# Kernel tuning notes

Hardware: AMD Instinct MI355X
Metric: run time of the kernel (lower is better)

Reference implementation:

```python
import jax, jax.numpy as jnp
import numpy as np
import math

B, N, DEG, C, F0, NCLS = 128, 512, 8, 128, 128, 10
E = B * N * DEG
RATIO = 0.8
K1 = math.ceil(RATIO * N)    # 410
K2 = math.ceil(RATIO * K1)   # 328
K3 = math.ceil(RATIO * K2)   # 263


def setup_inputs() -> dict:
    key = jax.random.key(0)
    ks = jax.random.split(key, 32)
    x = jax.random.normal(ks[0], (B * N, F0), jnp.float32)
    epg = N * DEG
    src_l = jax.random.randint(ks[1], (B, epg), 0, N)
    dst_l = jax.random.randint(ks[2], (B, epg), 0, N)
    off = (jnp.arange(B, dtype=jnp.int32) * N)[:, None]
    edge_src = (src_l + off).reshape(-1).astype(jnp.int32)
    edge_dst = (dst_l + off).reshape(-1).astype(jnp.int32)

    def lin(k, fi, fo):
        return jax.random.normal(k, (fi, fo), jnp.float32) / np.float32(np.sqrt(fi))

    inp = {"x": x, "edge_src": edge_src, "edge_dst": edge_dst}
    i = 3
    for s, fi in (("1", F0), ("2", C), ("3", C)):
        inp["Wroot" + s] = lin(ks[i], fi, C); i += 1
        inp["Wrel" + s] = lin(ks[i], fi, C); i += 1
        inp["brel" + s] = jnp.zeros((C,), jnp.float32)
        inp["p" + s] = jax.random.normal(ks[i], (C,), jnp.float32); i += 1
    inp["W1"] = lin(ks[i], 2 * C, 128); i += 1
    inp["b1"] = jnp.zeros((128,), jnp.float32)
    inp["W2"] = lin(ks[i], 128, 64); i += 1
    inp["b2"] = jnp.zeros((64,), jnp.float32)
    inp["W3"] = lin(ks[i], 64, NCLS); i += 1
    inp["b3"] = jnp.zeros((NCLS,), jnp.float32)
    return inp


def graph_conv(x, src, dst, emask, Wroot, Wrel, brel, num_nodes):
    # PyG GraphConv (aggr='add'): lin_rel(sum_j x_j) + lin_root(x_i)
    msg = x[src] * emask[:, None]                      # masked gather  [E, C]
    agg = jax.ops.segment_sum(msg, dst, num_segments=num_nodes)
    return agg @ Wrel + brel + x @ Wroot


def topk_pool(x, p, src, dst, emask, b, n, k):
    # score = tanh(x . p / ||p||), keep top-k nodes per graph, scale kept x by score
    score = jnp.tanh((x @ p) / jnp.linalg.norm(p))     # [b*n]
    vals, idx = jax.lax.top_k(score.reshape(b, n), k)  # [b, k]
    perm = (idx + (jnp.arange(b, dtype=idx.dtype) * n)[:, None]).reshape(-1)
    x_new = x[perm] * vals.reshape(-1, 1)
    inv = jnp.full((b * n,), -1, jnp.int32).at[perm].set(
        jnp.arange(b * k, dtype=jnp.int32))
    ns, nd = inv[src], inv[dst]
    nmask = emask * (ns >= 0) * (nd >= 0)
    return x_new, jnp.maximum(ns, 0), jnp.maximum(nd, 0), nmask


def readout(h, b, k):
    hb = h.reshape(b, k, -1)
    return jnp.concatenate([hb.max(axis=1), hb.mean(axis=1)], axis=-1)  # gmp||gap


def reference(x, edge_src, edge_dst,
              Wroot1, Wrel1, brel1, p1,
              Wroot2, Wrel2, brel2, p2,
              Wroot3, Wrel3, brel3, p3,
              W1, b1, W2, b2, W3, b3):
    emask = jnp.ones((E,), x.dtype)
    s, d = edge_src, edge_dst

    h = jax.nn.relu(graph_conv(x, s, d, emask, Wroot1, Wrel1, brel1, B * N))
    h, s, d, emask = topk_pool(h, p1, s, d, emask, B, N, K1)
    x1 = readout(h, B, K1)

    h = jax.nn.relu(graph_conv(h, s, d, emask, Wroot2, Wrel2, brel2, B * K1))
    h, s, d, emask = topk_pool(h, p2, s, d, emask, B, K1, K2)
    x2 = readout(h, B, K2)

    h = jax.nn.relu(graph_conv(h, s, d, emask, Wroot3, Wrel3, brel3, B * K2))
    h, s, d, emask = topk_pool(h, p3, s, d, emask, B, K2, K3)
    x3 = readout(h, B, K3)

    g = x1 + x2 + x3                                   # [B, 256]
    g = jax.nn.relu(g @ W1 + b1)                       # dropout is identity in eval
    g = jax.nn.relu(g @ W2 + b2)
    return jax.nn.log_softmax(g @ W3 + b3, axis=-1)    # [B, NCLS]
```

## Files before the change

kernel.cpp:

```cpp
#include <hip/hip_runtime.h>
#include <hip/hip_bf16.h>
#include <math.h>

#define B_G   128
#define N0    512
#define DEG   8
#define CCH   128
#define EPG   (N0*DEG)
#define E_TOTAL (B_G*EPG)
#define K1    410
#define K2    328
#define K3    263
#define NCLS  10

using bf16x8 = __attribute__((ext_vector_type(8))) __bf16;
using f32x4  = __attribute__((ext_vector_type(4))) float;
typedef unsigned short ushort;
typedef unsigned int uint;

__device__ __forceinline__ ushort f2b(float f) {
    uint u = __float_as_uint(f);
    u += 0x7fffu + ((u >> 16) & 1u);
    return (ushort)(u >> 16);
}
__device__ __forceinline__ float b2f(ushort h) {
    return __uint_as_float(((uint)h) << 16);
}
__device__ __forceinline__ void split2(float v, ushort& hi, ushort& lo) {
    hi = f2b(v);
    lo = f2b(v - b2f(hi));
}
__device__ __forceinline__ uint pksplit(float v) {
    ushort h, l; split2(v, h, l);
    return (uint)h | ((uint)l << 16);
}
__device__ __forceinline__ float unpk(uint u) {
    return __uint_as_float(u << 16) + __uint_as_float(u & 0xffff0000u);
}
__device__ __forceinline__ float keyval(unsigned long long key) {
    uint tu = (uint)(key >> 32);
    uint su = (tu & 0x80000000u) ? (tu & 0x7fffffffu) : ~tu;
    return __uint_as_float(su);
}

__global__ __launch_bounds__(512) void setup_kernel(
        const float* __restrict__ Wrel0, const float* __restrict__ Wroot0,
        const float* __restrict__ Wrel1, const float* __restrict__ Wroot1,
        const float* __restrict__ Wrel2, const float* __restrict__ Wroot2,
        ushort* __restrict__ Bph, ushort* __restrict__ Bpl,
        const int* __restrict__ es, const int* __restrict__ ed,
        int* __restrict__ indptr0, int* __restrict__ counts0, ushort* __restrict__ srclist0) {
    __shared__ uint epk[EPG];
    __shared__ int cnt[512], pref[512], curs[512];
    if (blockIdx.x < B_G) {
        int b = blockIdx.x, tid = threadIdx.x;
        cnt[tid] = 0;
        __syncthreads();
        int base = b * EPG;
        for (int i = tid; i < EPG; i += 512) {
            int s = es[base + i] & (N0 - 1);
            int d = ed[base + i] & (N0 - 1);
            epk[i] = (uint)s | ((uint)d << 16);
            atomicAdd(&cnt[d], 1);
        }
        __syncthreads();
        pref[tid] = cnt[tid];
        __syncthreads();
        for (int off = 1; off < 512; off <<= 1) {
            int v = (tid >= off) ? pref[tid - off] : 0;
            __syncthreads();
            pref[tid] += v;
            __syncthreads();
        }
        int excl = tid ? pref[tid - 1] : 0;
        indptr0[b * N0 + tid] = base + excl;
        counts0[b * N0 + tid] = cnt[tid];
        curs[tid] = excl;
        __syncthreads();
        for (int i = tid; i < EPG; i += 512) {
            uint wv = epk[i];
            int dl = wv >> 16;
            int pos = atomicAdd(&curs[dl], 1);
            srclist0[base + pos] = (ushort)(wv & 0xFFFFu);
        }
    } else {
        int i = (blockIdx.x - B_G) * 512 + threadIdx.x;
        if (i < 3 * 32768) {
            int layer = i >> 15, rem = i & 32767;
            int j = rem & 7, lane = (rem >> 3) & 63, cf = (rem >> 9) & 7, ks = rem >> 12;
            int k = ks * 32 + (lane >> 4) * 8 + j;
            int c = cf * 16 + (lane & 15);
            const float* Wrel  = layer == 0 ? Wrel0  : layer == 1 ? Wrel1  : Wrel2;
            const float* Wroot = layer == 0 ? Wroot0 : layer == 1 ? Wroot1 : Wroot2;
            float v = (k < 128) ? Wrel[k * 128 + c] : Wroot[(k - 128) * 128 + c];
            ushort hi, lo; split2(v, hi, lo);
            Bph[i] = hi; Bpl[i] = lo;
        }
    }
}

__global__ __launch_bounds__(1024) void aggregate0(
        const float* __restrict__ xf,
        const int* __restrict__ indptr, const int* __restrict__ counts,
        const ushort* __restrict__ srclist,
        uint* __restrict__ aggp) {
    extern __shared__ float slab[];
    int b = blockIdx.x >> 2, q = blockIdx.x & 3;
    int tid = threadIdx.x;
    const float4* xf4 = (const float4*)xf;
    for (int t = tid; t < N0 * 8; t += 1024) {
        int nd = t >> 3, c4 = t & 7;
        float4 u = xf4[(size_t)(b * N0 + nd) * 32 + q * 8 + c4];
        *(float4*)&slab[nd * 36 + c4 * 4] = u;
    }
    __syncthreads();
    int wave = tid >> 6, lane = tid & 63;
    int gl = lane >> 3, sub = lane & 7;
    for (int g = wave; g < N0 / 8; g += 16) {
        int d = g * 8 + gl;
        int beg = indptr[b * N0 + d];
        int cnt = counts[b * N0 + d];
        float4 acc = make_float4(0.f, 0.f, 0.f, 0.f);
        int id_next = (cnt > 0) ? (int)srclist[beg] : 0;
        for (int j = 0; j < cnt; j++) {
            int id = id_next;
            if (j + 1 < cnt) id_next = (int)srclist[beg + j + 1];
            const float4 v = *(const float4*)&slab[id * 36 + sub * 4];
            acc.x += v.x; acc.y += v.y; acc.z += v.z; acc.w += v.w;
        }
        uint4 o;
        o.x = pksplit(acc.x); o.y = pksplit(acc.y);
        o.z = pksplit(acc.z); o.w = pksplit(acc.w);
        *(uint4*)&aggp[(size_t)(b * N0 + d) * CCH + q * 32 + sub * 4] = o;
    }
}

__global__ __launch_bounds__(512, 4) void transform_mfma(
        const uint* __restrict__ aggp, const uint* __restrict__ hin,
        const float* __restrict__ rootf,
        const int* __restrict__ perm, const float* __restrict__ pval,
        const ushort* __restrict__ Bph, const ushort* __restrict__ Bpl,
        const float* __restrict__ brel, const float* __restrict__ pvec,
        uint* __restrict__ hout, float* __restrict__ score) {
    __shared__ ushort ldsBh[16384];
    __shared__ ushort ldsBl[16384];
    int tid = threadIdx.x;
    int wave = tid >> 6, lane = tid & 63;
    int r = lane & 15, kb = lane >> 4;
    int rows0 = blockIdx.x * 128 + wave * 16;
    int gid = rows0 + r;
    size_t oldrow = perm ? (size_t)perm[gid] : (size_t)gid;
    float rv = perm ? pval[gid] : 1.f;

    f32x4 acc[8];
#pragma unroll
    for (int cf = 0; cf < 8; cf++) acc[cf] = (f32x4)(0.f);

    union U16 { uint u[4]; bf16x8 v; };

#pragma unroll
    for (int half = 0; half < 2; half++) {
        if (half) __syncthreads();
#pragma unroll
        for (int i = 0; i < 4; i++) {
            int idx = tid + i * 512;
            ((uint4*)ldsBh)[idx] = ((const uint4*)(Bph + half * 16384))[idx];
            ((uint4*)ldsBl)[idx] = ((const uint4*)(Bpl + half * 16384))[idx];
        }
        __syncthreads();
#pragma unroll
        for (int ks4 = 0; ks4 < 4; ks4++) {
            U16 ah, al;
            if (half && rootf) {
                const float* R = rootf + (size_t)gid * CCH + ks4 * 32 + kb * 8;
                float4 f0 = *(const float4*)R;
                float4 f1 = *(const float4*)(R + 4);
                float c[8] = {f0.x, f0.y, f0.z, f0.w, f1.x, f1.y, f1.z, f1.w};
#pragma unroll
                for (int p2 = 0; p2 < 4; p2++) {
                    ushort h0, l0, h1, l1;
                    split2(c[2 * p2], h0, l0);
                    split2(c[2 * p2 + 1], h1, l1);
                    ah.u[p2] = (uint)h0 | ((uint)h1 << 16);
                    al.u[p2] = (uint)l0 | ((uint)l1 << 16);
                }
            } else {
                const uint* A = half ? hin : aggp;
                size_t abase = half ? oldrow * CCH : (size_t)gid * CCH;
                size_t rowbase = abase + ks4 * 32 + kb * 8;
                uint4 ua = *(const uint4*)&A[rowbase];
                uint4 ub = *(const uint4*)&A[rowbase + 4];
                if (half && perm) {
                    float c[8] = {unpk(ua.x) * rv, unpk(ua.y) * rv, unpk(ua.z) * rv,
                                  unpk(ua.w) * rv, unpk(ub.x) * rv, unpk(ub.y) * rv,
                                  unpk(ub.z) * rv, unpk(ub.w) * rv};
#pragma unroll
                    for (int p2 = 0; p2 < 4; p2++) {
                        ushort h0, l0, h1, l1;
                        split2(c[2 * p2], h0, l0);
                        split2(c[2 * p2 + 1], h1, l1);
                        ah.u[p2] = (uint)h0 | ((uint)h1 << 16);
                        al.u[p2] = (uint)l0 | ((uint)l1 << 16);
                    }
                } else {
                    ah.u[0] = (ua.x & 0xffffu) | (ua.y << 16);
                    ah.u[1] = (ua.z & 0xffffu) | (ua.w << 16);
                    ah.u[2] = (ub.x & 0xffffu) | (ub.y << 16);
                    ah.u[3] = (ub.z & 0xffffu) | (ub.w << 16);
                    al.u[0] = (ua.x >> 16) | (ua.y & 0xffff0000u);
                    al.u[1] = (ua.z >> 16) | (ua.w & 0xffff0000u);
                    al.u[2] = (ub.x >> 16) | (ub.y & 0xffff0000u);
                    al.u[3] = (ub.z >> 16) | (ub.w & 0xffff0000u);
                }
            }
#pragma unroll
            for (int cf = 0; cf < 8; cf++) {
                bf16x8 bh = *(const bf16x8*)&ldsBh[((ks4 * 8 + cf) * 64 + lane) * 8];
                bf16x8 bl = *(const bf16x8*)&ldsBl[((ks4 * 8 + cf) * 64 + lane) * 8];
                acc[cf] = __builtin_amdgcn_mfma_f32_16x16x32_bf16(ah.v, bl, acc[cf], 0, 0, 0);
                acc[cf] = __builtin_amdgcn_mfma_f32_16x16x32_bf16(al.v, bh, acc[cf], 0, 0, 0);
                acc[cf] = __builtin_amdgcn_mfma_f32_16x16x32_bf16(ah.v, bh, acc[cf], 0, 0, 0);
            }
        }
    }

    float pv[8], bb[8], q = 0.f;
#pragma unroll
    for (int cf = 0; cf < 8; cf++) {
        pv[cf] = pvec[cf * 16 + r];
        bb[cf] = brel[cf * 16 + r];
        q += pv[cf] * pv[cf];
    }
    float dots[4] = {0.f, 0.f, 0.f, 0.f};
#pragma unroll
    for (int cf = 0; cf < 8; cf++) {
#pragma unroll
        for (int reg = 0; reg < 4; reg++) {
            float v = acc[cf][reg] + bb[cf];
            v = v > 0.f ? v : 0.f;
            hout[(size_t)(rows0 + kb * 4 + reg) * CCH + cf * 16 + r] = pksplit(v);
            dots[reg] += v * pv[cf];
        }
    }
#pragma unroll
    for (int off = 1; off < 16; off <<= 1) {
        q += __shfl_xor(q, off);
#pragma unroll
        for (int reg = 0; reg < 4; reg++) dots[reg] += __shfl_xor(dots[reg], off);
    }
    if (r == 0) {
        float inv_norm = rsqrtf(q);
#pragma unroll
        for (int reg = 0; reg < 4; reg++)
            score[rows0 + kb * 4 + reg] = tanhf(dots[reg] * inv_norm);
    }
}

__global__ __launch_bounds__(512) void poolagg_kernel(
        const float* __restrict__ score, const uint* __restrict__ hp,
        int* __restrict__ perm_out, float* __restrict__ pval_out,
        float* __restrict__ gpart,
        const int* __restrict__ ipt_in, const int* __restrict__ cnt_in,
        const ushort* __restrict__ src_in,
        int* __restrict__ ipt_out, int* __restrict__ cnt_out,
        ushort* __restrict__ src_out,
        uint* __restrict__ aggout,
        int n, int k, int do_agg) {
    int b = blockIdx.x >> 2, q = blockIdx.x & 3;
    int tid = threadIdx.x;
    __shared__ unsigned long long keys[512];
    __shared__ short invl[512];
    __shared__ int cntL[512], prefL[512], iptL[512];
    __shared__ ushort srcL[EPG];
    extern __shared__ float slab[];
    {
        unsigned long long key = 0ull;
        if (tid < n) {
            uint u = __float_as_uint(score[b * n + tid]);
            u = (u & 0x80000000u) ? ~u : (u | 0x80000000u);
            key = ((unsigned long long)u << 32) | (uint)(~tid);
        }
        keys[tid] = key;
        invl[tid] = -1;
    }
    __syncthreads();
    for (int kk2 = 2; kk2 <= 512; kk2 <<= 1) {
        for (int j = kk2 >> 1; j > 0; j >>= 1) {
            int s = tid, sxj = s ^ j;
            if (sxj > s) {
                unsigned long long a = keys[s], c = keys[sxj];
                bool doSwap = ((s & kk2) == 0) ? (a < c) : (a > c);
                if (doSwap) { keys[s] = c; keys[sxj] = a; }
            }
            __syncthreads();
        }
    }
    if (tid < k) {
        int node = (int)(~(uint)keys[tid]);
        invl[node] = (short)tid;
    }
    __syncthreads();
    for (int t = tid; t < k * 8; t += 512) {
        int nd = t >> 3, c4 = t & 7;
        unsigned long long key = keys[nd];
        int node = (int)(~(uint)key);
        float v = keyval(key);
        uint4 u = *(const uint4*)&hp[(size_t)(b * n + node) * CCH + q * 32 + c4 * 4];
        *(float4*)&slab[nd * 36 + c4 * 4] =
            make_float4(unpk(u.x) * v, unpk(u.y) * v, unpk(u.z) * v, unpk(u.w) * v);
    }
    __syncthreads();
    {
        int ch = tid >> 4, w = tid & 15;
        float mx = -1e30f, sm = 0.f;
        for (int r2 = w; r2 < k; r2 += 16) {
            float v = slab[r2 * 36 + ch];
            mx = fmaxf(mx, v); sm += v;
        }
#pragma unroll
        for (int off = 1; off < 16; off <<= 1) {
            mx = fmaxf(mx, __shfl_xor(mx, off));
            sm += __shfl_xor(sm, off);
        }
        if (w == 0) {
            gpart[b * 256 + q * 32 + ch] = mx;
            gpart[b * 256 + 128 + q * 32 + ch] = sm / (float)k;
        }
    }
    if (!do_agg) return;
    int node = -1, beg = 0, c = 0, nk = 0;
    if (tid < k) {
        node = (int)(~(uint)keys[tid]);
        beg = ipt_in[b * n + node];
        c = cnt_in[b * n + node];
        for (int t = 0; t < c; t++)
            if (invl[src_in[beg + t]] >= 0) nk++;
    }
    cntL[tid] = (tid < k) ? nk : 0;
    __syncthreads();
    prefL[tid] = cntL[tid];
    __syncthreads();
    for (int off = 1; off < 512; off <<= 1) {
        int v = (tid >= off) ? prefL[tid - off] : 0;
        __syncthreads();
        prefL[tid] += v;
        __syncthreads();
    }
    int excl = tid ? prefL[tid - 1] : 0;
    iptL[tid] = excl;
    if (tid < k) {
        int pos = excl;
        for (int t = 0; t < c; t++) {
            int ns = invl[src_in[beg + t]];
            if (ns >= 0) srcL[pos++] = (ushort)ns;
        }
    }
    __syncthreads();
    if (q == 0) {
        int tot = prefL[511];
        if (tid < k) {
            ipt_out[b * k + tid] = b * EPG + excl;
            cnt_out[b * k + tid] = nk;
            perm_out[b * k + tid] = b * n + node;
            pval_out[b * k + tid] = keyval(keys[tid]);
        }
        for (int i = tid; i < tot; i += 512) src_out[b * EPG + i] = srcL[i];
    }
    {
        int wave = tid >> 6, lane = tid & 63;
        int gl = lane >> 3, sub = lane & 7;
        int ngroups = (k + 7) >> 3;
        for (int g = wave; g < ngroups; g += 8) {
            int d = g * 8 + gl;
            bool act = d < k;
            int bg = 0, cc = 0;
            if (act) { bg = iptL[d]; cc = cntL[d]; }
            float4 acc = make_float4(0.f, 0.f, 0.f, 0.f);
            for (int j = 0; j < cc; j++) {
                int id = (int)srcL[bg + j];
                const float4 v = *(const float4*)&slab[id * 36 + sub * 4];
                acc.x += v.x; acc.y += v.y; acc.z += v.z; acc.w += v.w;
            }
            if (act) {
                uint4 o;
                o.x = pksplit(acc.x); o.y = pksplit(acc.y);
                o.z = pksplit(acc.z); o.w = pksplit(acc.w);
                *(uint4*)&aggout[(size_t)(b * k + d) * CCH + q * 32 + sub * 4] = o;
            }
        }
    }
}

__global__ __launch_bounds__(128) void mlp_kernel(const float* __restrict__ gpart,
        const float* __restrict__ W1, const float* __restrict__ b1,
        const float* __restrict__ W2, const float* __restrict__ b2,
        const float* __restrict__ W3, const float* __restrict__ b3,
        float* __restrict__ out) {
    int b = blockIdx.x, t = threadIdx.x;
    __shared__ float gs[256], h1[128], h2[64], lg[10];
    const float* g0 = gpart + ((size_t)0 * B_G + b) * 256;
    const float* g1 = gpart + ((size_t)1 * B_G + b) * 256;
    const float* g2 = gpart + ((size_t)2 * B_G + b) * 256;
    gs[t] = g0[t] + g1[t] + g2[t];
    gs[128 + t] = g0[128 + t] + g1[128 + t] + g2[128 + t];
    __syncthreads();
    {
        float a = b1[t];
        for (int c = 0; c < 256; c++) a += gs[c] * W1[c * 128 + t];
        h1[t] = fmaxf(a, 0.f);
    }
    __syncthreads();
    if (t < 64) {
        float a = b2[t];
        for (int c = 0; c < 128; c++) a += h1[c] * W2[c * 64 + t];
        h2[t] = fmaxf(a, 0.f);
    }
    __syncthreads();
    if (t < 10) {
        float a = b3[t];
        for (int c = 0; c < 64; c++) a += h2[c] * W3[c * 10 + t];
        lg[t] = a;
    }
    __syncthreads();
    if (t < 10) {
        float m = lg[0];
        for (int i = 1; i < 10; i++) m = fmaxf(m, lg[i]);
        float s = 0.f;
        for (int i = 0; i < 10; i++) s += expf(lg[i] - m);
        out[b * 10 + t] = lg[t] - m - logf(s);
    }
}

extern "C" void kernel_launch(void* const* d_in, const int* in_sizes, int n_in,
                              void* d_out, int out_size, void* d_ws, size_t ws_size,
                              hipStream_t stream) {
    (void)in_sizes; (void)n_in; (void)out_size; (void)ws_size;
    const float* x0 = (const float*)d_in[0];
    const int* es = (const int*)d_in[1];
    const int* ed = (const int*)d_in[2];
    const float* Wroot[3] = {(const float*)d_in[3], (const float*)d_in[7], (const float*)d_in[11]};
    const float* Wrel[3]  = {(const float*)d_in[4], (const float*)d_in[8], (const float*)d_in[12]};
    const float* brel[3]  = {(const float*)d_in[5], (const float*)d_in[9], (const float*)d_in[13]};
    const float* pvec[3]  = {(const float*)d_in[6], (const float*)d_in[10], (const float*)d_in[14]};
    const float* W1 = (const float*)d_in[15];
    const float* b1 = (const float*)d_in[16];
    const float* W2 = (const float*)d_in[17];
    const float* b2 = (const float*)d_in[18];
    const float* W3 = (const float*)d_in[19];
    const float* b3 = (const float*)d_in[20];

    size_t off = 0;
    char* base = (char*)d_ws;
    auto alloc = [&](size_t bytes) -> void* {
        void* p = base + off;
        off += (bytes + 255) & ~(size_t)255;
        return p;
    };
    const size_t FEATP = (size_t)(B_G * N0) * CCH * 4;
    uint* P0 = (uint*)alloc(FEATP);
    uint* P1 = (uint*)alloc(FEATP);
    uint* P2 = (uint*)alloc(FEATP);
    ushort* Bph = (ushort*)alloc((size_t)3 * 32768 * 2);
    ushort* Bpl = (ushort*)alloc((size_t)3 * 32768 * 2);
    int* iptA = (int*)alloc((size_t)(B_G * N0) * 4);
    int* cntA = (int*)alloc((size_t)(B_G * N0) * 4);
    ushort* srcA = (ushort*)alloc((size_t)E_TOTAL * 2);
    int* iptB = (int*)alloc((size_t)(B_G * N0) * 4);
    int* cntB = (int*)alloc((size_t)(B_G * N0) * 4);
    ushort* srcB = (ushort*)alloc((size_t)E_TOTAL * 2);
    int* permA = (int*)alloc((size_t)(B_G * K1) * 4);
    float* pvalA = (float*)alloc((size_t)(B_G * K1) * 4);
    int* permB = (int*)alloc((size_t)(B_G * K1) * 4);
    float* pvalB = (float*)alloc((size_t)(B_G * K1) * 4);
    float* score = (float*)alloc((size_t)(B_G * N0) * 4);
    float* gpart = (float*)alloc((size_t)3 * B_G * 256 * 4);

    setup_kernel<<<B_G + (3 * 32768 + 511) / 512, 512, 0, stream>>>(
        Wrel[0], Wroot[0], Wrel[1], Wroot[1], Wrel[2], Wroot[2],
        Bph, Bpl, es, ed, iptA, cntA, srcA);

    aggregate0<<<4 * B_G, 1024, (size_t)N0 * 36 * 4, stream>>>(
        x0, iptA, cntA, srcA, P1);
    transform_mfma<<<B_G * N0 / 128, 512, 0, stream>>>(
        P1, nullptr, x0, nullptr, nullptr, Bph, Bpl, brel[0], pvec[0], P0, score);
    poolagg_kernel<<<4 * B_G, 512, (size_t)K1 * 36 * 4, stream>>>(
        score, P0, permA, pvalA, gpart + (size_t)0 * B_G * 256,
        iptA, cntA, srcA, iptB, cntB, srcB, P1, N0, K1, 1);

    transform_mfma<<<B_G * K1 / 128, 512, 0, stream>>>(
        P1, P0, nullptr, permA, pvalA, Bph + 32768, Bpl + 32768,
        brel[1], pvec[1], P2, score);
    poolagg_kernel<<<4 * B_G, 512, (size_t)K2 * 36 * 4, stream>>>(
        score, P2, permB, pvalB, gpart + (size_t)1 * B_G * 256,
        iptB, cntB, srcB, iptA, cntA, srcA, P1, K1, K2, 1);

    transform_mfma<<<B_G * K2 / 128, 512, 0, stream>>>(
        P1, P2, nullptr, permB, pvalB, Bph + 2 * 32768, Bpl + 2 * 32768,
        brel[2], pvec[2], P0, score);
    poolagg_kernel<<<4 * B_G, 512, (size_t)K3 * 36 * 4, stream>>>(
        score, P0, nullptr, nullptr, gpart + (size_t)2 * B_G * 256,
        iptA, cntA, srcA, nullptr, nullptr, nullptr, nullptr, K2, K3, 0);

    mlp_kernel<<<B_G, 128, 0, stream>>>(gpart, W1, b1, W2, b2, W3, b3, (float*)d_out);
}
```

Before: 195.5 us.

## Widen poolagg to 1024 threads, stage edge list in LDS, drop slab padding

The pool+aggregate kernel now runs 1024 threads per block. It copies the graph's incoming source list into shared memory before filtering, replacing repeated global reads. The readout max/mean uses a shared-memory cross-wave reduction instead of shuffles, the count/offset arrays are derived from the prefix buffer, and the gather loop prefetches the next index. The slab row stride drops from 36 to 32 floats in both aggregate kernels, which shrinks LDS use but may bring back bank conflicts. Many threads sit idle during the 512-element bitonic sort and scan, and per-block LDS rises, which may limit occupancy.

```diff
diff --git a/kernel.cpp b/kernel.cpp
--- a/kernel.cpp
+++ b/kernel.cpp
@@ -111,7 +111,7 @@
     for (int t = tid; t < N0 * 8; t += 1024) {
         int nd = t >> 3, c4 = t & 7;
         float4 u = xf4[(size_t)(b * N0 + nd) * 32 + q * 8 + c4];
-        *(float4*)&slab[nd * 36 + c4 * 4] = u;
+        *(float4*)&slab[nd * 32 + c4 * 4] = u;
     }
     __syncthreads();
     int wave = tid >> 6, lane = tid & 63;
@@ -125,7 +125,7 @@
         for (int j = 0; j < cnt; j++) {
             int id = id_next;
             if (j + 1 < cnt) id_next = (int)srclist[beg + j + 1];
-            const float4 v = *(const float4*)&slab[id * 36 + sub * 4];
+            const float4 v = *(const float4*)&slab[id * 32 + sub * 4];
             acc.x += v.x; acc.y += v.y; acc.z += v.z; acc.w += v.w;
         }
         uint4 o;
@@ -256,7 +256,7 @@
     }
 }
 
-__global__ __launch_bounds__(512) void poolagg_kernel(
+__global__ __launch_bounds__(1024) void poolagg_kernel(
         const float* __restrict__ score, const uint* __restrict__ hp,
         int* __restrict__ perm_out, float* __restrict__ pval_out,
         float* __restrict__ gpart,
@@ -270,10 +270,13 @@
     int tid = threadIdx.x;
     __shared__ unsigned long long keys[512];
     __shared__ short invl[512];
-    __shared__ int cntL[512], prefL[512], iptL[512];
-    __shared__ ushort srcL[EPG];
+    __shared__ int prefL[512];
+    __shared__ ushort srcIn[EPG];
+    __shared__ float wredbuf[2048];
+    ushort* srcOut = (ushort*)wredbuf;
     extern __shared__ float slab[];
-    {
+
+    if (tid < 512) {
         unsigned long long key = 0ull;
         if (tid < n) {
             uint u = __float_as_uint(score[b * n + tid]);
@@ -283,14 +286,21 @@
         keys[tid] = key;
         invl[tid] = -1;
     }
+    if (do_agg) {
+        const uint* s4 = (const uint*)(src_in + b * EPG);
+        uint* d4 = (uint*)srcIn;
+        for (int i = tid; i < EPG / 2; i += 1024) d4[i] = s4[i];
+    }
     __syncthreads();
     for (int kk2 = 2; kk2 <= 512; kk2 <<= 1) {
         for (int j = kk2 >> 1; j > 0; j >>= 1) {
-            int s = tid, sxj = s ^ j;
-            if (sxj > s) {
-                unsigned long long a = keys[s], c = keys[sxj];
-                bool doSwap = ((s & kk2) == 0) ? (a < c) : (a > c);
-                if (doSwap) { keys[s] = c; keys[sxj] = a; }
+            if (tid < 512) {
+                int s = tid, sxj = s ^ j;
+                if (sxj > s) {
+                    unsigned long long a = keys[s], c = keys[sxj];
+                    bool doSwap = ((s & kk2) == 0) ? (a < c) : (a > c);
+                    if (doSwap) { keys[s] = c; keys[sxj] = a; }
+                }
             }
             __syncthreads();
         }
@@ -300,59 +310,60 @@
         invl[node] = (short)tid;
     }
     __syncthreads();
-    for (int t = tid; t < k * 8; t += 512) {
+    for (int t = tid; t < k * 8; t += 1024) {
         int nd = t >> 3, c4 = t & 7;
         unsigned long long key = keys[nd];
         int node = (int)(~(uint)key);
         float v = keyval(key);
         uint4 u = *(const uint4*)&hp[(size_t)(b * n + node) * CCH + q * 32 + c4 * 4];
-        *(float4*)&slab[nd * 36 + c4 * 4] =
+        *(float4*)&slab[nd * 32 + c4 * 4] =
             make_float4(unpk(u.x) * v, unpk(u.y) * v, unpk(u.z) * v, unpk(u.w) * v);
     }
     __syncthreads();
     {
-        int ch = tid >> 4, w = tid & 15;
+        int w = tid >> 5, ch = tid & 31;
         float mx = -1e30f, sm = 0.f;
-        for (int r2 = w; r2 < k; r2 += 16) {
-            float v = slab[r2 * 36 + ch];
+        for (int r2 = w; r2 < k; r2 += 32) {
+            float v = slab[r2 * 32 + ch];
             mx = fmaxf(mx, v); sm += v;
         }
-#pragma unroll
-        for (int off = 1; off < 16; off <<= 1) {
-            mx = fmaxf(mx, __shfl_xor(mx, off));
-            sm += __shfl_xor(sm, off);
-        }
-        if (w == 0) {
-            gpart[b * 256 + q * 32 + ch] = mx;
-            gpart[b * 256 + 128 + q * 32 + ch] = sm / (float)k;
-        }
+        wredbuf[w * 32 + ch] = mx;
+        wredbuf[1024 + w * 32 + ch] = sm;
+    }
+    __syncthreads();
+    if (tid < 32) {
+        float m = -1e30f, s = 0.f;
+        for (int w = 0; w < 32; w++) {
+            m = fmaxf(m, wredbuf[w * 32 + tid]);
+            s += wredbuf[1024 + w * 32 + tid];
+        }
+        gpart[b * 256 + q * 32 + tid] = m;
+        gpart[b * 256 + 128 + q * 32 + tid] = s / (float)k;
     }
     if (!do_agg) return;
+    __syncthreads();
     int node = -1, beg = 0, c = 0, nk = 0;
     if (tid < k) {
         node = (int)(~(uint)keys[tid]);
-        beg = ipt_in[b * n + node];
+        beg = ipt_in[b * n + node] - b * EPG;
         c = cnt_in[b * n + node];
         for (int t = 0; t < c; t++)
-            if (invl[src_in[beg + t]] >= 0) nk++;
-    }
-    cntL[tid] = (tid < k) ? nk : 0;
-    __syncthreads();
-    prefL[tid] = cntL[tid];
+            if (invl[srcIn[beg + t]] >= 0) nk++;
+    }
+    if (tid < 512) prefL[tid] = (tid < k) ? nk : 0;
     __syncthreads();
     for (int off = 1; off < 512; off <<= 1) {
-        int v = (tid >= off) ? prefL[tid - off] : 0;
-        __syncthreads();
-        prefL[tid] += v;
-        __syncthreads();
-    }
-    int excl = tid ? prefL[tid - 1] : 0;
-    iptL[tid] = excl;
+        int v = (tid >= off && tid < 512) ? prefL[tid - off] : 0;
+        __syncthreads();
+        if (tid < 512) prefL[tid] += v;
+        __syncthreads();
+    }
+    int excl = (tid < 512 && tid) ? prefL[tid - 1] : 0;
     if (tid < k) {
         int pos = excl;
         for (int t = 0; t < c; t++) {
-            int ns = invl[src_in[beg + t]];
-            if (ns >= 0) srcL[pos++] = (ushort)ns;
+            int ns = invl[srcIn[beg + t]];
+            if (ns >= 0) srcOut[pos++] = (ushort)ns;
         }
     }
     __syncthreads();
@@ -364,21 +375,24 @@
             perm_out[b * k + tid] = b * n + node;
             pval_out[b * k + tid] = keyval(keys[tid]);
         }
-        for (int i = tid; i < tot; i += 512) src_out[b * EPG + i] = srcL[i];
+        for (int i = tid; i < tot; i += 1024) src_out[b * EPG + i] = srcOut[i];
     }
     {
         int wave = tid >> 6, lane = tid & 63;
         int gl = lane >> 3, sub = lane & 7;
         int ngroups = (k + 7) >> 3;
-        for (int g = wave; g < ngroups; g += 8) {
+        for (int g = wave; g < ngroups; g += 16) {
             int d = g * 8 + gl;
             bool act = d < k;
-            int bg = 0, cc = 0;
-            if (act) { bg = iptL[d]; cc = cntL[d]; }
+            int bg = 0, en = 0;
+            if (act) { bg = d ? prefL[d - 1] : 0; en = prefL[d]; }
+            int cc = en - bg;
             float4 acc = make_float4(0.f, 0.f, 0.f, 0.f);
+            int id_next = (cc > 0) ? (int)srcOut[bg] : 0;
             for (int j = 0; j < cc; j++) {
-                int id = (int)srcL[bg + j];
-                const float4 v = *(const float4*)&slab[id * 36 + sub * 4];
+                int id = id_next;
+                if (j + 1 < cc) id_next = (int)srcOut[bg + j + 1];
+                const float4 v = *(const float4*)&slab[id * 32 + sub * 4];
                 acc.x += v.x; acc.y += v.y; acc.z += v.z; acc.w += v.w;
             }
             if (act) {
@@ -479,25 +493,25 @@
         Wrel[0], Wroot[0], Wrel[1], Wroot[1], Wrel[2], Wroot[2],
         Bph, Bpl, es, ed, iptA, cntA, srcA);
 
-    aggregate0<<<4 * B_G, 1024, (size_t)N0 * 36 * 4, stream>>>(
+    aggregate0<<<4 * B_G, 1024, (size_t)N0 * 32 * 4, stream>>>(
         x0, iptA, cntA, srcA, P1);
     transform_mfma<<<B_G * N0 / 128, 512, 0, stream>>>(
         P1, nullptr, x0, nullptr, nullptr, Bph, Bpl, brel[0], pvec[0], P0, score);
-    poolagg_kernel<<<4 * B_G, 512, (size_t)K1 * 36 * 4, stream>>>(
+    poolagg_kernel<<<4 * B_G, 1024, (size_t)K1 * 32 * 4, stream>>>(
         score, P0, permA, pvalA, gpart + (size_t)0 * B_G * 256,
         iptA, cntA, srcA, iptB, cntB, srcB, P1, N0, K1, 1);
 
     transform_mfma<<<B_G * K1 / 128, 512, 0, stream>>>(
         P1, P0, nullptr, permA, pvalA, Bph + 32768, Bpl + 32768,
         brel[1], pvec[1], P2, score);
-    poolagg_kernel<<<4 * B_G, 512, (size_t)K2 * 36 * 4, stream>>>(
+    poolagg_kernel<<<4 * B_G, 1024, (size_t)K2 * 32 * 4, stream>>>(
         score, P2, permB, pvalB, gpart + (size_t)1 * B_G * 256,
         iptB, cntB, srcB, iptA, cntA, srcA, P1, K1, K2, 1);
 
     transform_mfma<<<B_G * K2 / 128, 512, 0, stream>>>(
         P1, P2, nullptr, permB, pvalB, Bph + 2 * 32768, Bpl + 2 * 32768,
         brel[2], pvec[2], P0, score);
-    poolagg_kernel<<<4 * B_G, 512, (size_t)K3 * 36 * 4, stream>>>(
+    poolagg_kernel<<<4 * B_G, 1024, (size_t)K3 * 32 * 4, stream>>>(
         score, P0, nullptr, nullptr, gpart + (size_t)2 * B_G * 256,
         iptA, cntA, srcA, nullptr, nullptr, nullptr, nullptr, K2, K3, 0);
 
```

Measured after the change: 197.5 us. No clear change (+1.0%).
